# Kernel optimization log

Hardware: AMD Instinct MI355X
Metric: run time of the kernel (lower is better)

## Reference

```python
import jax, jax.numpy as jnp
import numpy as np
import math

B, S, D, H = 4, 512, 128, 4
HD = D // H
NEG = float(-2**32 + 1)

def _ln(x, g, b, eps=1e-8):
    m = jnp.mean(x, axis=-1, keepdims=True)
    v = jnp.var(x, axis=-1, keepdims=True)
    return (x - m) * jax.lax.rsqrt(v + eps) * g + b

def setup_inputs() -> dict:
    key = jax.random.key(0)
    ks = jax.random.split(key, 16)
    s = 0.02
    inp = {
        'embed': jax.random.normal(ks[0], (B, S, D), jnp.float32),
        'time_matrix_K': jax.random.normal(ks[1], (B, S, S, D), jnp.float32),
        'time_matrix_V': jax.random.normal(ks[2], (B, S, S, D), jnp.float32),
        # causal additive mask: large negative above diagonal (1--mask semantics)
        'attn_mask': jnp.where(jnp.triu(jnp.ones((S, S), bool), k=1), jnp.float32(-1e9), jnp.float32(0.0)),
        'padding_mask': jnp.zeros((B, S), bool),
        'wq': jax.random.normal(ks[3], (D, D), jnp.float32) * s,
        'bq': jnp.zeros((D,), jnp.float32),
        'wk': jax.random.normal(ks[4], (D, D), jnp.float32) * s,
        'bk': jnp.zeros((D,), jnp.float32),
        'wv': jax.random.normal(ks[5], (D, D), jnp.float32) * s,
        'bv': jnp.zeros((D,), jnp.float32),
        'wo': jax.random.normal(ks[6], (D, D), jnp.float32) * s,
        'bo': jnp.zeros((D,), jnp.float32),
        'ln1_g': jnp.ones((D,), jnp.float32),
        'ln1_b': jnp.zeros((D,), jnp.float32),
        'ln2_g': jnp.ones((D,), jnp.float32),
        'ln2_b': jnp.zeros((D,), jnp.float32),
        'w1': jax.random.normal(ks[7], (D, D), jnp.float32) * s,  # d_ff defaults to d_model
        'b1': jnp.zeros((D,), jnp.float32),
        'w2': jax.random.normal(ks[8], (D, D), jnp.float32) * s,
        'b2': jnp.zeros((D,), jnp.float32),
    }
    return inp

def reference(embed, time_matrix_K, time_matrix_V, attn_mask, padding_mask,
              wq, bq, wk, bk, wv, bv, wo, bo,
              ln1_g, ln1_b, ln2_g, ln2_b, w1, b1, w2, b2):
    # Pre-LN on Q only (K, V take raw embed), per original block
    Qn = _ln(embed, ln1_g, ln1_b)
    q = (Qn @ wq + bq).reshape(B, S, H, HD).transpose(0, 2, 1, 3)      # bhqd
    k = (embed @ wk + bk).reshape(B, S, H, HD).transpose(0, 2, 1, 3)   # bhkd
    v = (embed @ wv + bv).reshape(B, S, H, HD).transpose(0, 2, 1, 3)   # bhkd
    tmK = time_matrix_K.reshape(B, S, S, H, HD).transpose(0, 3, 1, 2, 4)  # bhqkd
    tmV = time_matrix_V.reshape(B, S, S, H, HD).transpose(0, 3, 1, 2, 4)  # bhqkd
    scale = math.sqrt(HD)
    energy = jnp.einsum('bhqd,bhkd->bhqk', q, k)
    energy = energy + jnp.einsum('bhqkd,bhqd->bhqk', tmK, q)
    energy = energy / scale
    energy = energy + attn_mask[None, None]
    energy = jnp.where(padding_mask[:, None, None, :], jnp.float32(NEG), energy)
    attn = jax.nn.softmax(energy, axis=-1)  # dropout is identity in eval
    O = jnp.einsum('bhqk,bhkd->bhqd', attn, v)
    O = O + jnp.einsum('bhqk,bhqkd->bhqd', attn, tmV)
    O = O.transpose(0, 2, 1, 3).reshape(B, S, D)
    O = O @ wo + bo
    x = Qn + O                      # residual adds LN'd Q, per original code
    x = _ln(x, ln2_g, ln2_b)
    ff = jax.nn.gelu(x @ w1 + b1, approximate=False) @ w2 + b2
    return ff + x
```

## Files before the change

kernel.cpp:

```cpp
#include <hip/hip_runtime.h>
#include <math.h>

#define Bsz 4
#define Ssz 512
#define Dsz 128
#define Hsz 4
#define HDsz 32

typedef float floatx4 __attribute__((ext_vector_type(4)));

static __device__ __forceinline__ float4 ldnt4(const float* p) {
    floatx4 v = __builtin_nontemporal_load(reinterpret_cast<const floatx4*>(p));
    float4 r; r.x = v.x; r.y = v.y; r.z = v.z; r.w = v.w;
    return r;
}

__global__ __launch_bounds__(128) void k_pre(
    const float* __restrict__ embed,
    const float* __restrict__ wq, const float* __restrict__ bq,
    const float* __restrict__ wk, const float* __restrict__ bk,
    const float* __restrict__ wv, const float* __restrict__ bv,
    const float* __restrict__ g1, const float* __restrict__ b1,
    float* __restrict__ Qn, float* __restrict__ Qp,
    float* __restrict__ Kp, float* __restrict__ Vp)
{
    __shared__ float xs[4][128];
    __shared__ float qs[4][128];
    const int t = threadIdx.x;
    const int row0 = blockIdx.x * 4;
    const int r = t >> 5;
    const int c = t & 31;
    const int d4 = c << 2;

    const float4* e4 = (const float4*)(embed + (size_t)row0 * Dsz);
    float4 x4 = e4[r * 32 + c];

    float s = x4.x + x4.y + x4.z + x4.w;
    #pragma unroll
    for (int o = 1; o < 32; o <<= 1) s += __shfl_xor(s, o);
    const float m = s * (1.0f / 128.0f);

    const float dx0 = x4.x - m, dx1 = x4.y - m, dx2 = x4.z - m, dx3 = x4.w - m;
    float vs = dx0*dx0 + dx1*dx1 + dx2*dx2 + dx3*dx3;
    #pragma unroll
    for (int o = 1; o < 32; o <<= 1) vs += __shfl_xor(vs, o);
    const float rstd = rsqrtf(vs * (1.0f / 128.0f) + 1e-8f);

    const float4 g4 = *(const float4*)(g1 + d4);
    const float4 bb4 = *(const float4*)(b1 + d4);
    float4 qn4;
    qn4.x = dx0 * rstd * g4.x + bb4.x;
    qn4.y = dx1 * rstd * g4.y + bb4.y;
    qn4.z = dx2 * rstd * g4.z + bb4.z;
    qn4.w = dx3 * rstd * g4.w + bb4.w;

    xs[r][d4+0] = x4.x; xs[r][d4+1] = x4.y; xs[r][d4+2] = x4.z; xs[r][d4+3] = x4.w;
    qs[r][d4+0] = qn4.x; qs[r][d4+1] = qn4.y; qs[r][d4+2] = qn4.z; qs[r][d4+3] = qn4.w;
    *(float4*)(Qn + (size_t)(row0 + r) * Dsz + d4) = qn4;
    __syncthreads();

    float aq[4] = {0,0,0,0}, ak[4] = {0,0,0,0}, av[4] = {0,0,0,0};
    for (int d = 0; d < 128; ++d) {
        const float wqv = wq[d*128 + t];
        const float wkv = wk[d*128 + t];
        const float wvv = wv[d*128 + t];
        #pragma unroll
        for (int rr = 0; rr < 4; ++rr) {
            aq[rr] += qs[rr][d] * wqv;
            ak[rr] += xs[rr][d] * wkv;
            av[rr] += xs[rr][d] * wvv;
        }
    }
    const float bqv = bq[t], bkv = bk[t], bvv = bv[t];
    #pragma unroll
    for (int rr = 0; rr < 4; ++rr) {
        const size_t o = (size_t)(row0 + rr) * Dsz + t;
        Qp[o] = aq[rr] + bqv;
        Kp[o] = ak[rr] + bkv;
        Vp[o] = av[rr] + bvv;
    }
}

__global__ __launch_bounds__(256) void k_attn(
    const float* __restrict__ tmK, const float* __restrict__ tmV,
    const float* __restrict__ Qp, const float* __restrict__ Kp,
    const float* __restrict__ Vp,
    float* __restrict__ Oa)
{
    __shared__ float p_lds[Hsz][Ssz];
    __shared__ float qv[Dsz];
    __shared__ float invden[Hsz];
    __shared__ float red[8][32][4];

    const int t = threadIdx.x;
    const int idx = blockIdx.x >> 2;
    const int q = (idx & 1) ? (idx >> 1) : (Ssz - 1) - (idx >> 1);
    const int b = blockIdx.x & 3;
    const int nk = q + 1;
    const size_t rowq = (size_t)(b * Ssz + q);

    if (t < 128) qv[t] = Qp[rowq * Dsz + t];
    __syncthreads();

    const int kk_off = t >> 5;
    const int c = t & 31;
    const int d4 = c << 2;
    const int h = c >> 3;

    const float4 q4 = *(const float4*)(qv + d4);
    const float* tmKb = tmK + rowq * (size_t)Ssz * Dsz;
    const float* Kb = Kp + (size_t)b * Ssz * Dsz;
    const float inv_scale = 0.17677669529663687f;

    int k0 = 0;
    for (; k0 + 32 <= nk; k0 += 32) {
        float4 a[4], kv[4];
        #pragma unroll
        for (int u = 0; u < 4; ++u) {
            const int kk = k0 + kk_off + 8*u;
            a[u]  = ldnt4(tmKb + (size_t)kk * Dsz + d4);
            kv[u] = *(const float4*)(Kb + (size_t)kk * Dsz + d4);
        }
        #pragma unroll
        for (int u = 0; u < 4; ++u) {
            float val = q4.x*(a[u].x+kv[u].x) + q4.y*(a[u].y+kv[u].y)
                      + q4.z*(a[u].z+kv[u].z) + q4.w*(a[u].w+kv[u].w);
            val += __shfl_xor(val, 1);
            val += __shfl_xor(val, 2);
            val += __shfl_xor(val, 4);
            if ((c & 7) == 0) p_lds[h][k0 + kk_off + 8*u] = val * inv_scale;
        }
    }
    for (; k0 < nk; k0 += 8) {
        const int kk = k0 + kk_off;
        float val = 0.0f;
        if (kk < nk) {
            const float4 a  = ldnt4(tmKb + (size_t)kk * Dsz + d4);
            const float4 kv = *(const float4*)(Kb + (size_t)kk * Dsz + d4);
            val = q4.x*(a.x+kv.x) + q4.y*(a.y+kv.y) + q4.z*(a.z+kv.z) + q4.w*(a.w+kv.w);
        }
        val += __shfl_xor(val, 1);
        val += __shfl_xor(val, 2);
        val += __shfl_xor(val, 4);
        if ((c & 7) == 0 && kk < nk) p_lds[h][kk] = val * inv_scale;
    }
    __syncthreads();

    {
        const int hh = t >> 6;
        const int lane = t & 63;
        float mx = -INFINITY;
        for (int k = lane; k < nk; k += 64) mx = fmaxf(mx, p_lds[hh][k]);
        #pragma unroll
        for (int o = 1; o < 64; o <<= 1) mx = fmaxf(mx, __shfl_xor(mx, o));
        float ssum = 0.0f;
        for (int k = lane; k < nk; k += 64) {
            const float p = __expf(p_lds[hh][k] - mx);
            p_lds[hh][k] = p;
            ssum += p;
        }
        #pragma unroll
        for (int o = 1; o < 64; o <<= 1) ssum += __shfl_xor(ssum, o);
        if (lane == 0) invden[hh] = 1.0f / ssum;
    }
    __syncthreads();

    const float* tmVb = tmV + rowq * (size_t)Ssz * Dsz;
    const float* Vb = Vp + (size_t)b * Ssz * Dsz;
    float4 acc = {0.0f, 0.0f, 0.0f, 0.0f};
    k0 = 0;
    for (; k0 + 32 <= nk; k0 += 32) {
        float4 a[4], vv[4];
        #pragma unroll
        for (int u = 0; u < 4; ++u) {
            const int kk = k0 + kk_off + 8*u;
            a[u]  = ldnt4(tmVb + (size_t)kk * Dsz + d4);
            vv[u] = *(const float4*)(Vb + (size_t)kk * Dsz + d4);
        }
        #pragma unroll
        for (int u = 0; u < 4; ++u) {
            const float p = p_lds[h][k0 + kk_off + 8*u];
            acc.x += p * (a[u].x + vv[u].x);
            acc.y += p * (a[u].y + vv[u].y);
            acc.z += p * (a[u].z + vv[u].z);
            acc.w += p * (a[u].w + vv[u].w);
        }
    }
    for (; k0 < nk; k0 += 8) {
        const int kk = k0 + kk_off;
        if (kk < nk) {
            const float p = p_lds[h][kk];
            const float4 a  = ldnt4(tmVb + (size_t)kk * Dsz + d4);
            const float4 vv = *(const float4*)(Vb + (size_t)kk * Dsz + d4);
            acc.x += p * (a.x + vv.x);
            acc.y += p * (a.y + vv.y);
            acc.z += p * (a.z + vv.z);
            acc.w += p * (a.w + vv.w);
        }
    }
    red[kk_off][c][0] = acc.x;
    red[kk_off][c][1] = acc.y;
    red[kk_off][c][2] = acc.z;
    red[kk_off][c][3] = acc.w;
    __syncthreads();
    if (t < 128) {
        const int cc = t >> 2, j = t & 3;
        float ssum = 0.0f;
        #pragma unroll
        for (int g = 0; g < 8; ++g) ssum += red[g][cc][j];
        Oa[rowq * Dsz + t] = ssum * invden[t >> 5];
    }
}

__global__ __launch_bounds__(128) void k_post(
    const float* __restrict__ Oa, const float* __restrict__ Qn,
    const float* __restrict__ wo, const float* __restrict__ bo,
    const float* __restrict__ g2, const float* __restrict__ b2ln,
    const float* __restrict__ w1, const float* __restrict__ b1,
    const float* __restrict__ w2, const float* __restrict__ b2,
    float* __restrict__ out)
{
    __shared__ float os[4][128];
    __shared__ float xn[4][128];
    __shared__ float hbuf[4][128];
    const int t = threadIdx.x;
    const int row0 = blockIdx.x * 4;
    const int r = t >> 5;
    const int c = t & 31;
    const int d4 = c << 2;

    {
        const float4* o4 = (const float4*)(Oa + (size_t)row0 * Dsz);
        const float4 v = o4[r * 32 + c];
        os[r][d4+0] = v.x; os[r][d4+1] = v.y; os[r][d4+2] = v.z; os[r][d4+3] = v.w;
    }
    __syncthreads();

    float ao[4] = {0,0,0,0};
    for (int d = 0; d < 128; ++d) {
        const float wv = wo[d*128 + t];
        #pragma unroll
        for (int rr = 0; rr < 4; ++rr) ao[rr] += os[rr][d] * wv;
    }
    const float bov = bo[t];
    float xrow[4];
    #pragma unroll
    for (int rr = 0; rr < 4; ++rr)
        xrow[rr] = Qn[(size_t)(row0 + rr) * Dsz + t] + ao[rr] + bov;
    __syncthreads();
    #pragma unroll
    for (int rr = 0; rr < 4; ++rr) os[rr][t] = xrow[rr];
    __syncthreads();

    {
        const float4 x4 = *(const float4*)(&os[r][d4]);
        float s = x4.x + x4.y + x4.z + x4.w;
        #pragma unroll
        for (int o = 1; o < 32; o <<= 1) s += __shfl_xor(s, o);
        const float m = s * (1.0f / 128.0f);
        const float dx0 = x4.x - m, dx1 = x4.y - m, dx2 = x4.z - m, dx3 = x4.w - m;
        float vs = dx0*dx0 + dx1*dx1 + dx2*dx2 + dx3*dx3;
        #pragma unroll
        for (int o = 1; o < 32; o <<= 1) vs += __shfl_xor(vs, o);
        const float rstd = rsqrtf(vs * (1.0f / 128.0f) + 1e-8f);
        const float4 g4 = *(const float4*)(g2 + d4);
        const float4 bb4 = *(const float4*)(b2ln + d4);
        xn[r][d4+0] = dx0 * rstd * g4.x + bb4.x;
        xn[r][d4+1] = dx1 * rstd * g4.y + bb4.y;
        xn[r][d4+2] = dx2 * rstd * g4.z + bb4.z;
        xn[r][d4+3] = dx3 * rstd * g4.w + bb4.w;
    }
    __syncthreads();

    float a1[4] = {0,0,0,0};
    for (int d = 0; d < 128; ++d) {
        const float wv = w1[d*128 + t];
        #pragma unroll
        for (int rr = 0; rr < 4; ++rr) a1[rr] += xn[rr][d] * wv;
    }
    const float b1v = b1[t];
    #pragma unroll
    for (int rr = 0; rr < 4; ++rr) {
        const float hv = a1[rr] + b1v;
        hbuf[rr][t] = 0.5f * hv * (1.0f + erff(hv * 0.70710678118654752f));
    }
    __syncthreads();

    float a2[4] = {0,0,0,0};
    for (int d = 0; d < 128; ++d) {
        const float wv = w2[d*128 + t];
        #pragma unroll
        for (int rr = 0; rr < 4; ++rr) a2[rr] += hbuf[rr][d] * wv;
    }
    const float b2v = b2[t];
    #pragma unroll
    for (int rr = 0; rr < 4; ++rr)
        out[(size_t)(row0 + rr) * Dsz + t] = a2[rr] + b2v + xn[rr][t];
}

extern "C" void kernel_launch(void* const* d_in, const int* in_sizes, int n_in,
                              void* d_out, int out_size, void* d_ws, size_t ws_size,
                              hipStream_t stream) {
    const float* embed = (const float*)d_in[0];
    const float* tmK   = (const float*)d_in[1];
    const float* tmV   = (const float*)d_in[2];
    const float* wq = (const float*)d_in[5];
    const float* bq = (const float*)d_in[6];
    const float* wk = (const float*)d_in[7];
    const float* bk = (const float*)d_in[8];
    const float* wv = (const float*)d_in[9];
    const float* bv = (const float*)d_in[10];
    const float* wo = (const float*)d_in[11];
    const float* bo = (const float*)d_in[12];
    const float* g1 = (const float*)d_in[13];
    const float* b1l = (const float*)d_in[14];
    const float* g2 = (const float*)d_in[15];
    const float* b2l = (const float*)d_in[16];
    const float* w1 = (const float*)d_in[17];
    const float* b1 = (const float*)d_in[18];
    const float* w2 = (const float*)d_in[19];
    const float* b2 = (const float*)d_in[20];

    const size_t NE = (size_t)Bsz * Ssz * Dsz;
    float* ws = (float*)d_ws;
    float* Qn = ws;
    float* Qp = ws + NE;
    float* Kp = ws + 2 * NE;
    float* Vp = ws + 3 * NE;
    float* Oa = ws + 4 * NE;

    k_pre<<<(Bsz * Ssz) / 4, 128, 0, stream>>>(embed, wq, bq, wk, bk, wv, bv,
                                               g1, b1l, Qn, Qp, Kp, Vp);
    k_attn<<<Bsz * Ssz, 256, 0, stream>>>(tmK, tmV, Qp, Kp, Vp, Oa);
    k_post<<<(Bsz * Ssz) / 4, 128, 0, stream>>>(Oa, Qn, wo, bo, g2, b2l,
                                                w1, b1, w2, b2, (float*)d_out);
}
```

Before: 164.8 us.

## Split attention over key tiles with partial softmax and combine kernel

Splits each query row's causal attention into 64-key tiles handled by separate blocks, each writing a partial output plus max and sum. A new combine kernel merges the tiles with log-sum-exp rescaling. This is meant to improve load balance and parallelism across the triangular workload. In exchange it launches many blocks that exit immediately, adds a kernel launch, and writes and reads partial buffers from a larger workspace.

```diff
diff --git a/kernel.cpp b/kernel.cpp
--- a/kernel.cpp
+++ b/kernel.cpp
@@ -6,6 +6,8 @@
 #define Dsz 128
 #define Hsz 4
 #define HDsz 32
+#define KT 64
+#define NT 8
 
 typedef float floatx4 __attribute__((ext_vector_type(4)));
 
@@ -81,22 +83,27 @@
     }
 }
 
-__global__ __launch_bounds__(256) void k_attn(
+__global__ __launch_bounds__(256) void k_attn_tile(
     const float* __restrict__ tmK, const float* __restrict__ tmV,
     const float* __restrict__ Qp, const float* __restrict__ Kp,
     const float* __restrict__ Vp,
-    float* __restrict__ Oa)
+    float* __restrict__ Opart,
+    float* __restrict__ ml)
 {
-    __shared__ float p_lds[Hsz][Ssz];
+    __shared__ float p_lds[Hsz][KT];
     __shared__ float qv[Dsz];
-    __shared__ float invden[Hsz];
     __shared__ float red[8][32][4];
 
+    const int id = blockIdx.x;
+    const int b = id & 3;
+    const int q = (id >> 2) & (Ssz - 1);
+    const int tile = id >> 11;
+    const int k0 = tile * KT;
+    if (k0 > q) return;
+
     const int t = threadIdx.x;
-    const int idx = blockIdx.x >> 2;
-    const int q = (idx & 1) ? (idx >> 1) : (Ssz - 1) - (idx >> 1);
-    const int b = blockIdx.x & 3;
-    const int nk = q + 1;
+    const int nr_full = q - k0 + 1;
+    const int nr = nr_full > KT ? KT : nr_full;
     const size_t rowq = (size_t)(b * Ssz + q);
 
     if (t < 128) qv[t] = Qp[rowq * Dsz + t];
@@ -108,16 +115,16 @@
     const int h = c >> 3;
 
     const float4 q4 = *(const float4*)(qv + d4);
-    const float* tmKb = tmK + rowq * (size_t)Ssz * Dsz;
-    const float* Kb = Kp + (size_t)b * Ssz * Dsz;
+    const float* tmKb = tmK + (rowq * (size_t)Ssz + k0) * Dsz;
+    const float* Kb   = Kp + ((size_t)b * Ssz + k0) * Dsz;
     const float inv_scale = 0.17677669529663687f;
 
-    int k0 = 0;
-    for (; k0 + 32 <= nk; k0 += 32) {
+    int kr = 0;
+    for (; kr + 32 <= nr; kr += 32) {
         float4 a[4], kv[4];
         #pragma unroll
         for (int u = 0; u < 4; ++u) {
-            const int kk = k0 + kk_off + 8*u;
+            const int kk = kr + kk_off + 8*u;
             a[u]  = ldnt4(tmKb + (size_t)kk * Dsz + d4);
             kv[u] = *(const float4*)(Kb + (size_t)kk * Dsz + d4);
         }
@@ -128,13 +135,13 @@
             val += __shfl_xor(val, 1);
             val += __shfl_xor(val, 2);
             val += __shfl_xor(val, 4);
-            if ((c & 7) == 0) p_lds[h][k0 + kk_off + 8*u] = val * inv_scale;
-        }
-    }
-    for (; k0 < nk; k0 += 8) {
-        const int kk = k0 + kk_off;
+            if ((c & 7) == 0) p_lds[h][kr + kk_off + 8*u] = val * inv_scale;
+        }
+    }
+    for (; kr < nr; kr += 8) {
+        const int kk = kr + kk_off;
         float val = 0.0f;
-        if (kk < nk) {
+        if (kk < nr) {
             const float4 a  = ldnt4(tmKb + (size_t)kk * Dsz + d4);
             const float4 kv = *(const float4*)(Kb + (size_t)kk * Dsz + d4);
             val = q4.x*(a.x+kv.x) + q4.y*(a.y+kv.y) + q4.z*(a.z+kv.z) + q4.w*(a.w+kv.w);
@@ -142,7 +149,7 @@
         val += __shfl_xor(val, 1);
         val += __shfl_xor(val, 2);
         val += __shfl_xor(val, 4);
-        if ((c & 7) == 0 && kk < nk) p_lds[h][kk] = val * inv_scale;
+        if ((c & 7) == 0 && kk < nr) p_lds[h][kk] = val * inv_scale;
     }
     __syncthreads();
 
@@ -150,45 +157,49 @@
         const int hh = t >> 6;
         const int lane = t & 63;
         float mx = -INFINITY;
-        for (int k = lane; k < nk; k += 64) mx = fmaxf(mx, p_lds[hh][k]);
+        if (lane < nr) mx = p_lds[hh][lane];
         #pragma unroll
         for (int o = 1; o < 64; o <<= 1) mx = fmaxf(mx, __shfl_xor(mx, o));
-        float ssum = 0.0f;
-        for (int k = lane; k < nk; k += 64) {
-            const float p = __expf(p_lds[hh][k] - mx);
-            p_lds[hh][k] = p;
-            ssum += p;
-        }
+        float p = 0.0f;
+        if (lane < nr) {
+            p = __expf(p_lds[hh][lane] - mx);
+            p_lds[hh][lane] = p;
+        }
+        float ssum = p;
         #pragma unroll
         for (int o = 1; o < 64; o <<= 1) ssum += __shfl_xor(ssum, o);
-        if (lane == 0) invden[hh] = 1.0f / ssum;
-    }
-    __syncthreads();
-
-    const float* tmVb = tmV + rowq * (size_t)Ssz * Dsz;
-    const float* Vb = Vp + (size_t)b * Ssz * Dsz;
+        if (lane == 0) {
+            float* mlp = ml + ((rowq * NT + tile) * Hsz + hh) * 2;
+            mlp[0] = mx;
+            mlp[1] = ssum;
+        }
+    }
+    __syncthreads();
+
+    const float* tmVb = tmV + (rowq * (size_t)Ssz + k0) * Dsz;
+    const float* Vb   = Vp + ((size_t)b * Ssz + k0) * Dsz;
     float4 acc = {0.0f, 0.0f, 0.0f, 0.0f};
-    k0 = 0;
-    for (; k0 + 32 <= nk; k0 += 32) {
+    kr = 0;
+    for (; kr + 32 <= nr; kr += 32) {
         float4 a[4], vv[4];
         #pragma unroll
         for (int u = 0; u < 4; ++u) {
-            const int kk = k0 + kk_off + 8*u;
+            const int kk = kr + kk_off + 8*u;
             a[u]  = ldnt4(tmVb + (size_t)kk * Dsz + d4);
             vv[u] = *(const float4*)(Vb + (size_t)kk * Dsz + d4);
         }
         #pragma unroll
         for (int u = 0; u < 4; ++u) {
-            const float p = p_lds[h][k0 + kk_off + 8*u];
+            const float p = p_lds[h][kr + kk_off + 8*u];
             acc.x += p * (a[u].x + vv[u].x);
             acc.y += p * (a[u].y + vv[u].y);
             acc.z += p * (a[u].z + vv[u].z);
             acc.w += p * (a[u].w + vv[u].w);
         }
     }
-    for (; k0 < nk; k0 += 8) {
-        const int kk = k0 + kk_off;
-        if (kk < nk) {
+    for (; kr < nr; kr += 8) {
+        const int kk = kr + kk_off;
+        if (kk < nr) {
             const float p = p_lds[h][kk];
             const float4 a  = ldnt4(tmVb + (size_t)kk * Dsz + d4);
             const float4 vv = *(const float4*)(Vb + (size_t)kk * Dsz + d4);
@@ -208,8 +219,34 @@
         float ssum = 0.0f;
         #pragma unroll
         for (int g = 0; g < 8; ++g) ssum += red[g][cc][j];
-        Oa[rowq * Dsz + t] = ssum * invden[t >> 5];
-    }
+        Opart[(rowq * NT + tile) * Dsz + t] = ssum;
+    }
+}
+
+__global__ __launch_bounds__(128) void k_combine(
+    const float* __restrict__ Opart, const float* __restrict__ ml,
+    float* __restrict__ Oa)
+{
+    const size_t rowq = blockIdx.x;
+    const int q = (int)(rowq & (Ssz - 1));
+    const int nt = (q >> 6) + 1;
+    const int d = threadIdx.x;
+    const int h = d >> 5;
+
+    float M = -INFINITY;
+    #pragma unroll 8
+    for (int i = 0; i < nt; ++i)
+        M = fmaxf(M, ml[((rowq * NT + i) * Hsz + h) * 2 + 0]);
+
+    float den = 0.0f, o = 0.0f;
+    #pragma unroll 8
+    for (int i = 0; i < nt; ++i) {
+        const float* mlp = ml + ((rowq * NT + i) * Hsz + h) * 2;
+        const float w = __expf(mlp[0] - M);
+        den += w * mlp[1];
+        o   += w * Opart[(rowq * NT + i) * Dsz + d];
+    }
+    Oa[rowq * Dsz + d] = o / den;
 }
 
 __global__ __launch_bounds__(128) void k_post(
@@ -328,10 +365,14 @@
     float* Kp = ws + 2 * NE;
     float* Vp = ws + 3 * NE;
     float* Oa = ws + 4 * NE;
+    float* Opart = ws + 5 * NE;
+    float* mlbuf = ws + 5 * NE + (size_t)Bsz * Ssz * NT * Dsz;
 
     k_pre<<<(Bsz * Ssz) / 4, 128, 0, stream>>>(embed, wq, bq, wk, bk, wv, bv,
                                                g1, b1l, Qn, Qp, Kp, Vp);
-    k_attn<<<Bsz * Ssz, 256, 0, stream>>>(tmK, tmV, Qp, Kp, Vp, Oa);
+    k_attn_tile<<<Bsz * Ssz * NT, 256, 0, stream>>>(tmK, tmV, Qp, Kp, Vp,
+                                                    Opart, mlbuf);
+    k_combine<<<Bsz * Ssz, 128, 0, stream>>>(Opart, mlbuf, Oa);
     k_post<<<(Bsz * Ssz) / 4, 128, 0, stream>>>(Oa, Qn, wo, bo, g2, b2l,
                                                 w1, b1, w2, b2, (float*)d_out);
 }
```

Result: faster. 144.6 us (-12.3%).
